# Kernel tuning notes

Hardware: AMD Instinct MI355X
Metric: run time of the kernel (lower is better)

## Reference

```python
import jax, jax.numpy as jnp
import numpy as np

DIM = 33
BATCH, W, H = 8, 1024, 1024


def _identity_lut(dim):
    # Matches IdentityLUT33.txt: flat index n = i*dim^2 + j*dim + k holds
    # (r, g, b) = (k, j, i)/(dim-1), i.e. r varies fastest.
    g = jnp.arange(dim, dtype=jnp.float32) / (dim - 1)
    lut = jnp.stack([
        jnp.broadcast_to(g[None, None, :], (dim, dim, dim)),  # R channel
        jnp.broadcast_to(g[None, :, None], (dim, dim, dim)),  # G channel
        jnp.broadcast_to(g[:, None, None], (dim, dim, dim)),  # B channel
    ])
    return lut  # [3, dim, dim, dim]


def setup_inputs() -> dict:
    key = jax.random.key(0)
    LUT = _identity_lut(DIM)
    x = jax.random.uniform(key, (BATCH, 3, W, H), dtype=jnp.float32)
    return {"LUT": LUT, "x": x}


def reference(LUT, x):
    # x: [B, 3, W, H] with values in [0, 1]; LUT: [3, dim, dim, dim]
    dim = LUT.shape[-1]
    binsize = 1.0001 / (dim - 1)  # guarantees floor index <= dim-2 for x <= 1
    scaled = x / binsize
    idx = jnp.floor(scaled).astype(jnp.int32)   # bin indices per channel
    frac = scaled - idx                          # trilinear fractions
    r0, g0, b0 = idx[:, 0], idx[:, 1], idx[:, 2]   # each [B, W, H]
    rd, gd, bd = frac[:, 0], frac[:, 1], frac[:, 2]

    def corner(dr, dg, db):
        # CUDA kernel: flat id = r + g*dim + b*dim^2 within each channel,
        # so [3,d,d,d] LUT is indexed LUT[c, b, g, r]. Result: [3, B, W, H].
        return LUT[:, b0 + db, g0 + dg, r0 + dr]

    out = (((1 - rd) * (1 - gd) * (1 - bd))[None] * corner(0, 0, 0)
           + (rd * (1 - gd) * (1 - bd))[None] * corner(1, 0, 0)
           + ((1 - rd) * gd * (1 - bd))[None] * corner(0, 1, 0)
           + (rd * gd * (1 - bd))[None] * corner(1, 1, 0)
           + ((1 - rd) * (1 - gd) * bd)[None] * corner(0, 0, 1)
           + (rd * (1 - gd) * bd)[None] * corner(1, 0, 1)
           + ((1 - rd) * gd * bd)[None] * corner(0, 1, 1)
           + (rd * gd * bd)[None] * corner(1, 1, 1))
    return jnp.transpose(out, (1, 0, 2, 3))  # [B, 3, W, H]
```

## Files before the change

### kernel.cpp

```cpp
#include <hip/hip_runtime.h>


namespace {

constexpr int DIM    = 33;
constexpr int WH     = 1024 * 1024;
constexpr int BATCH  = 8;
constexpr int NPIX   = BATCH * WH;
constexpr int LUT_N  = DIM * DIM * DIM;

constexpr int BLOCKS  = 256;
constexpr int TPB     = 1024;
constexpr int NTHREAD = BLOCKS * TPB;
constexpr int NGROUP  = NPIX / 4;
constexpr int NITER   = NGROUP / NTHREAD;

using f4 = __attribute__((ext_vector_type(4))) float;

__device__ __forceinline__ f4 nt_load4(const float* p) {
    return __builtin_nontemporal_load((const f4*)p);
}
__device__ __forceinline__ void st4(float* p, f4 v) {
    *(f4*)p = v;
}

struct Gath {
    unsigned int q0, q1, q2, q3, q4, q5, q6, q7;
    float fr, fg, fb;
};

__device__ __forceinline__ Gath gather_px(
    const unsigned int* lds_lut, float r, float g, float b)
{
    const float inv_binsize = 32.0f / 1.0001f;
    float sr = r * inv_binsize;
    float sg = g * inv_binsize;
    float sb = b * inv_binsize;
    int ir = (int)sr, ig = (int)sg, ib = (int)sb;

    Gath G;
    G.fr = sr - (float)ir;
    G.fg = sg - (float)ig;
    G.fb = sb - (float)ib;

    int base  = ib * (DIM * DIM) + ig * DIM + ir;
    int base2 = base + DIM * DIM;
    G.q0 = lds_lut[base];
    G.q1 = lds_lut[base + 1];
    G.q2 = lds_lut[base + DIM];
    G.q3 = lds_lut[base + DIM + 1];
    G.q4 = lds_lut[base2];
    G.q5 = lds_lut[base2 + 1];
    G.q6 = lds_lut[base2 + DIM];
    G.q7 = lds_lut[base2 + DIM + 1];
    return G;
}

__device__ __forceinline__ void math_px(
    const Gath& G, float& outR, float& outG, float& outB)
{
    float fr = G.fr, fg = G.fg, fb = G.fb;
    float w00 = (1.f - fg) * (1.f - fb);
    float w10 = fg * (1.f - fb);
    float w01 = (1.f - fg) * fb;
    float w11 = fg * fb;
    float w000 = (1.f - fr) * w00, w100 = fr * w00;
    float w010 = (1.f - fr) * w10, w110 = fr * w10;
    float w001 = (1.f - fr) * w01, w101 = fr * w01;
    float w011 = (1.f - fr) * w11, w111 = fr * w11;

    float accR, accG, accB;
    accR  = w000 * (float)(G.q0 & 1023u);
    accG  = w000 * (float)((G.q0 >> 10) & 1023u);
    accB  = w000 * (float)((G.q0 >> 20) & 1023u);
    accR += w100 * (float)(G.q1 & 1023u);
    accG += w100 * (float)((G.q1 >> 10) & 1023u);
    accB += w100 * (float)((G.q1 >> 20) & 1023u);
    accR += w010 * (float)(G.q2 & 1023u);
    accG += w010 * (float)((G.q2 >> 10) & 1023u);
    accB += w010 * (float)((G.q2 >> 20) & 1023u);
    accR += w110 * (float)(G.q3 & 1023u);
    accG += w110 * (float)((G.q3 >> 10) & 1023u);
    accB += w110 * (float)((G.q3 >> 20) & 1023u);
    accR += w001 * (float)(G.q4 & 1023u);
    accG += w001 * (float)((G.q4 >> 10) & 1023u);
    accB += w001 * (float)((G.q4 >> 20) & 1023u);
    accR += w101 * (float)(G.q5 & 1023u);
    accG += w101 * (float)((G.q5 >> 10) & 1023u);
    accB += w101 * (float)((G.q5 >> 20) & 1023u);
    accR += w011 * (float)(G.q6 & 1023u);
    accG += w011 * (float)((G.q6 >> 10) & 1023u);
    accB += w011 * (float)((G.q6 >> 20) & 1023u);
    accR += w111 * (float)(G.q7 & 1023u);
    accG += w111 * (float)((G.q7 >> 10) & 1023u);
    accB += w111 * (float)((G.q7 >> 20) & 1023u);

    const float inv1023 = 1.0f / 1023.0f;
    outR = accR * inv1023;
    outG = accG * inv1023;
    outB = accB * inv1023;
}

__global__ __launch_bounds__(TPB, 1) void lut3d_lds_kernel(
    const float* __restrict__ lut, const float* __restrict__ x,
    float* __restrict__ out)
{
    __shared__ unsigned int lds_lut[LUT_N];

    const int tid = threadIdx.x;
    int gid = blockIdx.x * TPB + tid;

    int P = gid * 4;
    int batch = P >> 20;
    int p = P & (WH - 1);
    const float* xb = x + (size_t)batch * 3 * WH + p;
    f4 r4 = nt_load4(xb);
    f4 g4 = nt_load4(xb + WH);
    f4 b4 = nt_load4(xb + 2 * WH);

#pragma unroll
    for (int k = 0; k < 35; ++k) {
        int i = tid + k * TPB;
        float r = lut[i];
        float g = lut[LUT_N + i];
        float b = lut[2 * LUT_N + i];
        unsigned int qr = (unsigned int)__float2int_rn(__saturatef(r) * 1023.0f);
        unsigned int qg = (unsigned int)__float2int_rn(__saturatef(g) * 1023.0f);
        unsigned int qb = (unsigned int)__float2int_rn(__saturatef(b) * 1023.0f);
        lds_lut[i] = qr | (qg << 10) | (qb << 20);
    }
    if (tid < LUT_N - 35 * TPB) {
        int i = tid + 35 * TPB;
        float r = lut[i];
        float g = lut[LUT_N + i];
        float b = lut[2 * LUT_N + i];
        unsigned int qr = (unsigned int)__float2int_rn(__saturatef(r) * 1023.0f);
        unsigned int qg = (unsigned int)__float2int_rn(__saturatef(g) * 1023.0f);
        unsigned int qb = (unsigned int)__float2int_rn(__saturatef(b) * 1023.0f);
        lds_lut[i] = qr | (qg << 10) | (qb << 20);
    }
    __syncthreads();

#pragma unroll
    for (int it = 0; it < NITER; ++it) {
        float* ob = out + (size_t)batch * 3 * WH + p;

        int gn = gid + NTHREAD;
        int Pn = gn * 4;
        int batchN = Pn >> 20;
        int pN = Pn & (WH - 1);
        const float* xn = x + (size_t)batchN * 3 * WH + pN;
        const bool pf = (it + 1 < NITER);
        f4 rn = r4, gnv = g4, bn = b4;

        Gath A = gather_px(lds_lut, r4[0], g4[0], b4[0]);
        if (pf) rn = nt_load4(xn);
        Gath B = gather_px(lds_lut, r4[1], g4[1], b4[1]);

        f4 oR, oG, oB;
        { float tR, tG, tB; math_px(A, tR, tG, tB); oR[0]=tR; oG[0]=tG; oB[0]=tB; }
        if (pf) gnv = nt_load4(xn + WH);
        Gath C = gather_px(lds_lut, r4[2], g4[2], b4[2]);
        { float tR, tG, tB; math_px(B, tR, tG, tB); oR[1]=tR; oG[1]=tG; oB[1]=tB; }
        if (pf) bn = nt_load4(xn + 2 * WH);
        Gath D = gather_px(lds_lut, r4[3], g4[3], b4[3]);
        { float tR, tG, tB; math_px(C, tR, tG, tB); oR[2]=tR; oG[2]=tG; oB[2]=tB; }
        { float tR, tG, tB; math_px(D, tR, tG, tB); oR[3]=tR; oG[3]=tG; oB[3]=tB; }

        st4(ob,          oR);
        st4(ob + WH,     oG);
        st4(ob + 2 * WH, oB);

        gid = gn; batch = batchN; p = pN;
        r4 = rn; g4 = gnv; b4 = bn;
    }
}

}

extern "C" void kernel_launch(void* const* d_in, const int* in_sizes, int n_in,
                              void* d_out, int out_size, void* d_ws, size_t ws_size,
                              hipStream_t stream) {
    const float* lut = (const float*)d_in[0];
    const float* x   = (const float*)d_in[1];
    float*       out = (float*)d_out;
    (void)d_ws; (void)ws_size;

    lut3d_lds_kernel<<<BLOCKS, TPB, 0, stream>>>(lut, x, out);
}
```

Measured before the change: 183.4 us.

## Deepen input prefetch to two iterations and simplify per-iteration addressing

Loads of pixel inputs now run two iterations ahead using a double-buffered register array, rather than one iteration ahead interleaved with the gathers. Address math collapses to a fixed base plus it*3*WH because each iteration covers exactly one batch image. The blue-channel mask is removed since the top bits are known to be zero. The launch bounds minimum blocks hint changes from 1 to 4, which constrains register allocation even though LDS use (about 144 KB per block) likely limits residency anyway. The deeper prefetch costs more live registers and may raise register pressure.

```diff
diff --git a/kernel.cpp b/kernel.cpp
--- a/kernel.cpp
+++ b/kernel.cpp
@@ -12,8 +12,8 @@
 constexpr int BLOCKS  = 256;
 constexpr int TPB     = 1024;
 constexpr int NTHREAD = BLOCKS * TPB;
-constexpr int NGROUP  = NPIX / 4;
-constexpr int NITER   = NGROUP / NTHREAD;
+constexpr int NITER   = NPIX / 4 / NTHREAD;
+static_assert(NTHREAD * 4 == WH, "address collapse relies on this");
 
 using f4 = __attribute__((ext_vector_type(4))) float;
 
@@ -72,28 +72,28 @@
     float accR, accG, accB;
     accR  = w000 * (float)(G.q0 & 1023u);
     accG  = w000 * (float)((G.q0 >> 10) & 1023u);
-    accB  = w000 * (float)((G.q0 >> 20) & 1023u);
+    accB  = w000 * (float)(G.q0 >> 20);
     accR += w100 * (float)(G.q1 & 1023u);
     accG += w100 * (float)((G.q1 >> 10) & 1023u);
-    accB += w100 * (float)((G.q1 >> 20) & 1023u);
+    accB += w100 * (float)(G.q1 >> 20);
     accR += w010 * (float)(G.q2 & 1023u);
     accG += w010 * (float)((G.q2 >> 10) & 1023u);
-    accB += w010 * (float)((G.q2 >> 20) & 1023u);
+    accB += w010 * (float)(G.q2 >> 20);
     accR += w110 * (float)(G.q3 & 1023u);
     accG += w110 * (float)((G.q3 >> 10) & 1023u);
-    accB += w110 * (float)((G.q3 >> 20) & 1023u);
+    accB += w110 * (float)(G.q3 >> 20);
     accR += w001 * (float)(G.q4 & 1023u);
     accG += w001 * (float)((G.q4 >> 10) & 1023u);
-    accB += w001 * (float)((G.q4 >> 20) & 1023u);
+    accB += w001 * (float)(G.q4 >> 20);
     accR += w101 * (float)(G.q5 & 1023u);
     accG += w101 * (float)((G.q5 >> 10) & 1023u);
-    accB += w101 * (float)((G.q5 >> 20) & 1023u);
+    accB += w101 * (float)(G.q5 >> 20);
     accR += w011 * (float)(G.q6 & 1023u);
     accG += w011 * (float)((G.q6 >> 10) & 1023u);
-    accB += w011 * (float)((G.q6 >> 20) & 1023u);
+    accB += w011 * (float)(G.q6 >> 20);
     accR += w111 * (float)(G.q7 & 1023u);
     accG += w111 * (float)((G.q7 >> 10) & 1023u);
-    accB += w111 * (float)((G.q7 >> 20) & 1023u);
+    accB += w111 * (float)(G.q7 >> 20);
 
     const float inv1023 = 1.0f / 1023.0f;
     outR = accR * inv1023;
@@ -101,22 +101,25 @@
     outB = accB * inv1023;
 }
 
-__global__ __launch_bounds__(TPB, 1) void lut3d_lds_kernel(
+__global__ __launch_bounds__(TPB, 4) void lut3d_lds_kernel(
     const float* __restrict__ lut, const float* __restrict__ x,
     float* __restrict__ out)
 {
     __shared__ unsigned int lds_lut[LUT_N];
 
     const int tid = threadIdx.x;
-    int gid = blockIdx.x * TPB + tid;
+    const int gid = blockIdx.x * TPB + tid;
+    const int p0  = gid * 4;
+    const float* xp = x + p0;
+    float*       op = out + p0;
 
-    int P = gid * 4;
-    int batch = P >> 20;
-    int p = P & (WH - 1);
-    const float* xb = x + (size_t)batch * 3 * WH + p;
-    f4 r4 = nt_load4(xb);
-    f4 g4 = nt_load4(xb + WH);
-    f4 b4 = nt_load4(xb + 2 * WH);
+    f4 R[2], G[2], B[2];
+    R[0] = nt_load4(xp);
+    G[0] = nt_load4(xp + WH);
+    B[0] = nt_load4(xp + 2 * WH);
+    R[1] = nt_load4(xp + 3 * WH);
+    G[1] = nt_load4(xp + 4 * WH);
+    B[1] = nt_load4(xp + 5 * WH);
 
 #pragma unroll
     for (int k = 0; k < 35; ++k) {
@@ -143,36 +146,31 @@
 
 #pragma unroll
     for (int it = 0; it < NITER; ++it) {
-        float* ob = out + (size_t)batch * 3 * WH + p;
+        const int s = it & 1;
+        f4 r4 = R[s], g4 = G[s], b4 = B[s];
 
-        int gn = gid + NTHREAD;
-        int Pn = gn * 4;
-        int batchN = Pn >> 20;
-        int pN = Pn & (WH - 1);
-        const float* xn = x + (size_t)batchN * 3 * WH + pN;
-        const bool pf = (it + 1 < NITER);
-        f4 rn = r4, gnv = g4, bn = b4;
+        if (it + 2 < NITER) {
+            const float* xn = xp + (size_t)(it + 2) * 3 * WH;
+            R[s] = nt_load4(xn);
+            G[s] = nt_load4(xn + WH);
+            B[s] = nt_load4(xn + 2 * WH);
+        }
 
-        Gath A = gather_px(lds_lut, r4[0], g4[0], b4[0]);
-        if (pf) rn = nt_load4(xn);
-        Gath B = gather_px(lds_lut, r4[1], g4[1], b4[1]);
+        Gath A  = gather_px(lds_lut, r4[0], g4[0], b4[0]);
+        Gath Bg = gather_px(lds_lut, r4[1], g4[1], b4[1]);
+        Gath C  = gather_px(lds_lut, r4[2], g4[2], b4[2]);
 
         f4 oR, oG, oB;
-        { float tR, tG, tB; math_px(A, tR, tG, tB); oR[0]=tR; oG[0]=tG; oB[0]=tB; }
-        if (pf) gnv = nt_load4(xn + WH);
-        Gath C = gather_px(lds_lut, r4[2], g4[2], b4[2]);
-        { float tR, tG, tB; math_px(B, tR, tG, tB); oR[1]=tR; oG[1]=tG; oB[1]=tB; }
-        if (pf) bn = nt_load4(xn + 2 * WH);
-        Gath D = gather_px(lds_lut, r4[3], g4[3], b4[3]);
-        { float tR, tG, tB; math_px(C, tR, tG, tB); oR[2]=tR; oG[2]=tG; oB[2]=tB; }
-        { float tR, tG, tB; math_px(D, tR, tG, tB); oR[3]=tR; oG[3]=tG; oB[3]=tB; }
+        { float tR, tG, tB; math_px(A,  tR, tG, tB); oR[0]=tR; oG[0]=tG; oB[0]=tB; }
+        Gath D  = gather_px(lds_lut, r4[3], g4[3], b4[3]);
+        { float tR, tG, tB; math_px(Bg, tR, tG, tB); oR[1]=tR; oG[1]=tG; oB[1]=tB; }
+        { float tR, tG, tB; math_px(C,  tR, tG, tB); oR[2]=tR; oG[2]=tG; oB[2]=tB; }
+        { float tR, tG, tB; math_px(D,  tR, tG, tB); oR[3]=tR; oG[3]=tG; oB[3]=tB; }
 
+        float* ob = op + (size_t)it * 3 * WH;
         st4(ob,          oR);
         st4(ob + WH,     oG);
         st4(ob + 2 * WH, oB);
-
-        gid = gn; batch = batchN; p = pN;
-        r4 = rn; g4 = gnv; b4 = bn;
     }
 }
 
```

Measured after the change: 182.0 us. No clear change (-0.8%).
